# Performance work log

Hardware: AMD Instinct MI355X
Metric: run time of the kernel (lower is better)

The kernel has to match this reference:

```python
import jax, jax.numpy as jnp
import numpy as np

B, T, D = 2, 2048, 2048
N, K, H = 8, 4, 256
WINDOW = 1024
BASE_FREQ = 10000
ROPE_PROP = 1.0
SCALE_FACTOR = 1.0
K_MASK = -2.3819763e+38


def apply_rope(inputs, positions, base_frequency, scale_factor=1.0, rope_proportion=1.0):
    # inputs: [B,L,N,H], positions: [B,L]
    head_dim = inputs.shape[-1]
    rope_angles = int(rope_proportion * head_dim // 2)
    nope_angles = head_dim // 2 - rope_angles
    freq_exponents = 2.0 / head_dim * jnp.arange(rope_angles, dtype=jnp.float32)
    timescale = jnp.pad(base_frequency ** freq_exponents, (0, nope_angles),
                        mode='constant', constant_values=(0, jnp.inf))
    sinusoid = positions[..., None].astype(jnp.float32) / timescale[None, None, :]
    sinusoid = sinusoid[..., None, :] / scale_factor  # [B,L,1,H//2]
    sin = jnp.sin(sinusoid)
    cos = jnp.cos(sinusoid)
    first, second = jnp.split(inputs, 2, axis=-1)
    out = jnp.concatenate([first * cos - second * sin,
                           second * cos + first * sin], axis=-1)
    return out.astype(inputs.dtype)


def rms_norm(x, scale, eps=1e-6):
    var = jnp.mean(jnp.square(x.astype(jnp.float32)), axis=-1, keepdims=True)
    normed = x * jax.lax.rsqrt(var + eps)
    return (normed * (1.0 + scale)).astype(x.dtype)


def setup_inputs() -> dict:
    key = jax.random.key(0)
    ks = jax.random.split(key, 5)
    std = 0.02
    return {
        'x': jax.random.normal(ks[0], (B, T, D), jnp.float32),
        'positions': jnp.broadcast_to(jnp.arange(T, dtype=jnp.int32), (B, T)),
        'q_w': jax.random.normal(ks[1], (N, D, H), jnp.float32) * std,
        'k_w': jax.random.normal(ks[2], (K, D, H), jnp.float32) * std,
        'v_w': jax.random.normal(ks[3], (K, D, H), jnp.float32) * std,
        'o_w': jax.random.normal(ks[4], (N, H, D), jnp.float32) * std,
        'q_norm_scale': jnp.zeros((H,), jnp.float32),
        'k_norm_scale': jnp.zeros((H,), jnp.float32),
    }


def reference(x, positions, q_w, k_w, v_w, o_w, q_norm_scale, k_norm_scale):
    # QKV projections (Einsum modules)
    q = jnp.einsum('btd,ndh->btnh', x, q_w)   # [B,T,N,H]
    k = jnp.einsum('bsd,kdh->bskh', x, k_w)   # [B,S,K,H]
    v = jnp.einsum('bsd,kdh->bskh', x, v_w)
    # QK RMSNorm (gemma-style, zero-centered scale)
    q = rms_norm(q, q_norm_scale)
    k = rms_norm(k, k_norm_scale)
    # RoPE (local attention: base 10000, full proportion)
    q = apply_rope(q, positions, BASE_FREQ, SCALE_FACTOR, ROPE_PROP)
    k = apply_rope(k, positions, BASE_FREQ, SCALE_FACTOR, ROPE_PROP)
    q = q * (H ** -0.5)
    # GQA: group queries over kv heads
    G = N // K
    qg = q.reshape(B, T, K, G, H)
    logits = jnp.einsum('btkgh,bskh->btkgs', qg, k)  # [B,T,K,G,S]
    # causal + sliding-window mask from positions
    qp = positions[:, :, None]
    kp = positions[:, None, :]
    mask = (kp <= qp) & (kp > qp - WINDOW)           # [B,T,S]
    logits = jnp.where(mask[:, :, None, None, :], logits, K_MASK)
    probs = jax.nn.softmax(logits.astype(jnp.float32), axis=-1).astype(logits.dtype)
    out = jnp.einsum('btkgs,bskh->btkgh', probs, v).reshape(B, T, N, H)
    return jnp.einsum('btnh,nhd->btd', out, o_w)
```

## Files before the change

kernel.cpp:

```cpp
#include <hip/hip_runtime.h>
#include <cmath>

#define T_SEQ 2048
#define WINDOW 1024

typedef __attribute__((ext_vector_type(8))) short bf16x8;
typedef __attribute__((ext_vector_type(4))) float f32x4;
typedef __attribute__((ext_vector_type(16))) float f32x16;

__device__ __forceinline__ unsigned short f2bf(float f) {
  union { float f; unsigned int u; } v; v.f = f;
  unsigned int r = v.u + 0x7FFFu + ((v.u >> 16) & 1u);
  return (unsigned short)(r >> 16);
}
__device__ __forceinline__ float bf2f(unsigned short u) {
  union { unsigned int i; float f; } v; v.i = ((unsigned int)u) << 16;
  return v.f;
}

#define GLD16(gp, lp)                                                  \
  __builtin_amdgcn_global_load_lds(                                    \
      (__attribute__((address_space(1))) unsigned int*)(gp),           \
      (__attribute__((address_space(3))) unsigned int*)(lp), 16, 0, 0)

__global__ __launch_bounds__(256) void prep(
    const float* __restrict__ x,
    const float* __restrict__ qw, const float* __restrict__ kw,
    const float* __restrict__ vw, const float* __restrict__ ow,
    unsigned short* __restrict__ xb, unsigned short* __restrict__ wqkvt,
    unsigned short* __restrict__ wot) {
  __shared__ float tile[64][65];
  const int blk = blockIdx.x;
  const int tid = threadIdx.x;
  if (blk < 8192) {
    size_t i = (size_t)blk * 256 + tid;
    float4 v = *(const float4*)&x[i * 4];
    ushort4 o;
    o.x = f2bf(v.x); o.y = f2bf(v.y); o.z = f2bf(v.z); o.w = f2bf(v.w);
    *(ushort4*)&xb[i * 4] = o;
    return;
  }
  int tx = tid & 15, ty = tid >> 4;
  if (blk < 10240) {
    int idx = blk - 8192;
    int c0 = (idx & 63) * 64, d0 = (idx >> 6) * 64;
    const float* src; int hbase;
    if (c0 < 2048) { src = qw + (size_t)(c0 >> 8) * 524288; hbase = c0 & 255; }
    else if (c0 < 3072) { int cc = c0 - 2048; src = kw + (size_t)(cc >> 8) * 524288; hbase = cc & 255; }
    else { int cc = c0 - 3072; src = vw + (size_t)(cc >> 8) * 524288; hbase = cc & 255; }
#pragma unroll
    for (int p = 0; p < 4; ++p) {
      float4 v = *(const float4*)&src[(size_t)(d0 + ty + 16 * p) * 256 + hbase + tx * 4];
      tile[ty + 16 * p][tx * 4 + 0] = v.x; tile[ty + 16 * p][tx * 4 + 1] = v.y;
      tile[ty + 16 * p][tx * 4 + 2] = v.z; tile[ty + 16 * p][tx * 4 + 3] = v.w;
    }
    __syncthreads();
#pragma unroll
    for (int p = 0; p < 4; ++p) {
      int hh = ty + 16 * p;
      ushort4 o;
      o.x = f2bf(tile[tx * 4 + 0][hh]); o.y = f2bf(tile[tx * 4 + 1][hh]);
      o.z = f2bf(tile[tx * 4 + 2][hh]); o.w = f2bf(tile[tx * 4 + 3][hh]);
      *(ushort4*)&wqkvt[(size_t)(c0 + hh) * 2048 + d0 + tx * 4] = o;
    }
  } else {
    int idx = blk - 10240;
    int j0 = (idx & 31) * 64, d0 = (idx >> 5) * 64;
#pragma unroll
    for (int p = 0; p < 4; ++p) {
      float4 v = *(const float4*)&ow[(size_t)(j0 + ty + 16 * p) * 2048 + d0 + tx * 4];
      tile[ty + 16 * p][tx * 4 + 0] = v.x; tile[ty + 16 * p][tx * 4 + 1] = v.y;
      tile[ty + 16 * p][tx * 4 + 2] = v.z; tile[ty + 16 * p][tx * 4 + 3] = v.w;
    }
    __syncthreads();
#pragma unroll
    for (int p = 0; p < 4; ++p) {
      int hh = ty + 16 * p;
      ushort4 o;
      o.x = f2bf(tile[tx * 4 + 0][hh]); o.y = f2bf(tile[tx * 4 + 1][hh]);
      o.z = f2bf(tile[tx * 4 + 2][hh]); o.w = f2bf(tile[tx * 4 + 3][hh]);
      *(ushort4*)&wot[(size_t)(d0 + hh) * 2048 + j0 + tx * 4] = o;
    }
  }
}

__global__ __launch_bounds__(512) void gemm_qkv_256(
    const unsigned short* __restrict__ xb, const unsigned short* __restrict__ wt,
    unsigned short* __restrict__ qo, unsigned short* __restrict__ ko,
    unsigned short* __restrict__ vo) {
  __shared__ unsigned short lds[65536];
  const int tid = threadIdx.x;
  const int wave = tid >> 6, lane = tid & 63;
  const int wr = wave >> 2, wc = wave & 3;
  const int fm = lane & 15, fk = lane >> 4;

  const int bid = blockIdx.x;
  const int swz = (bid & 7) * 32 + (bid >> 3);
  const int m0 = (swz >> 4) * 256, n0 = (swz & 15) * 256;

  const int soff = fm * 32 + ((fk ^ ((fm >> 2) & 3)) << 3);
  const int aoff = wr * 4096 + soff;
  const int boff = wc * 2048 + soff;

  const unsigned short* Ab = xb + (size_t)m0 * 2048;
  const unsigned short* Bb = wt + (size_t)n0 * 2048;

  const int l0 = tid, l1 = tid + 512;
  const int r0 = l0 >> 2, o0 = l0 & 3;
  const int r1 = l1 >> 2, o1 = l1 & 3;
  const int sA0 = r0 * 2048 + ((o0 ^ ((r0 >> 2) & 3)) << 3);
  const int sA1 = r1 * 2048 + ((o1 ^ ((r1 >> 2) & 3)) << 3);

#define STAGE(srcbase, kofs, dstbase)                  \
  do {                                                 \
    GLD16((srcbase) + sA0 + (kofs), (dstbase) + l0 * 8); \
    GLD16((srcbase) + sA1 + (kofs), (dstbase) + l1 * 8); \
  } while (0)

  f32x4 acc[8][4];
#pragma unroll
  for (int i = 0; i < 8; ++i)
#pragma unroll
    for (int j = 0; j < 4; ++j) acc[i][j] = {0.f, 0.f, 0.f, 0.f};

  STAGE(Ab, 0,  lds + 0);
  STAGE(Bb, 0,  lds + 16384);
  STAGE(Ab, 32, lds + 8192);
  STAGE(Bb, 32, lds + 24576);
  STAGE(Ab, 64, lds + 32768);
  STAGE(Bb, 64, lds + 49152);
  asm volatile("s_waitcnt vmcnt(8)" ::: "memory");
  __builtin_amdgcn_s_barrier();

  for (int t = 0; t < 32; ++t) {
    const int p = t & 1;
    unsigned short* base = lds + p * 32768;
    unsigned short* xbase = lds + (p ^ 1) * 32768;
    const int t1 = (t < 31) ? t + 1 : 31;
    const int t2 = (t < 30) ? t + 2 : 31;

    bf16x8 a[4], b[4];
#pragma unroll
    for (int i = 0; i < 4; ++i) a[i] = *(const bf16x8*)(base + aoff + i * 512);
#pragma unroll
    for (int j = 0; j < 4; ++j) b[j] = *(const bf16x8*)(base + 16384 + boff + j * 512);
    STAGE(Ab, t1 * 64 + 32, xbase + 8192);
    __builtin_amdgcn_s_barrier();
    asm volatile("s_waitcnt lgkmcnt(0)" ::: "memory");
    __builtin_amdgcn_sched_barrier(0);
    __builtin_amdgcn_s_setprio(1);
#pragma unroll
    for (int i = 0; i < 4; ++i)
#pragma unroll
      for (int j = 0; j < 4; ++j)
        acc[i][j] = __builtin_amdgcn_mfma_f32_16x16x32_bf16(a[i], b[j], acc[i][j], 0, 0, 0);
    __builtin_amdgcn_s_setprio(0);
    __builtin_amdgcn_s_barrier();

#pragma unroll
    for (int i = 0; i < 4; ++i) a[i] = *(const bf16x8*)(base + aoff + (i + 4) * 512);
    STAGE(Bb, t1 * 64 + 32, xbase + 24576);
    __builtin_amdgcn_s_barrier();
    asm volatile("s_waitcnt lgkmcnt(0)" ::: "memory");
    __builtin_amdgcn_sched_barrier(0);
    __builtin_amdgcn_s_setprio(1);
#pragma unroll
    for (int i = 0; i < 4; ++i)
#pragma unroll
      for (int j = 0; j < 4; ++j)
        acc[i + 4][j] = __builtin_amdgcn_mfma_f32_16x16x32_bf16(a[i], b[j], acc[i + 4][j], 0, 0, 0);
    __builtin_amdgcn_s_setprio(0);
    asm volatile("s_waitcnt vmcnt(8)" ::: "memory");
    __builtin_amdgcn_s_barrier();

#pragma unroll
    for (int i = 0; i < 4; ++i) a[i] = *(const bf16x8*)(base + 8192 + aoff + i * 512);
#pragma unroll
    for (int j = 0; j < 4; ++j) b[j] = *(const bf16x8*)(base + 24576 + boff + j * 512);
    STAGE(Ab, t2 * 64, base + 0);
    __builtin_amdgcn_s_barrier();
    asm volatile("s_waitcnt lgkmcnt(0)" ::: "memory");
    __builtin_amdgcn_sched_barrier(0);
    __builtin_amdgcn_s_setprio(1);
#pragma unroll
    for (int i = 0; i < 4; ++i)
#pragma unroll
      for (int j = 0; j < 4; ++j)
        acc[i][j] = __builtin_amdgcn_mfma_f32_16x16x32_bf16(a[i], b[j], acc[i][j], 0, 0, 0);
    __builtin_amdgcn_s_setprio(0);
    __builtin_amdgcn_s_barrier();

#pragma unroll
    for (int i = 0; i < 4; ++i) a[i] = *(const bf16x8*)(base + 8192 + aoff + (i + 4) * 512);
    STAGE(Bb, t2 * 64, base + 16384);
    __builtin_amdgcn_s_barrier();
    asm volatile("s_waitcnt lgkmcnt(0)" ::: "memory");
    __builtin_amdgcn_sched_barrier(0);
    __builtin_amdgcn_s_setprio(1);
#pragma unroll
    for (int i = 0; i < 4; ++i)
#pragma unroll
      for (int j = 0; j < 4; ++j)
        acc[i + 4][j] = __builtin_amdgcn_mfma_f32_16x16x32_bf16(a[i], b[j], acc[i + 4][j], 0, 0, 0);
    __builtin_amdgcn_s_setprio(0);
    asm volatile("s_waitcnt vmcnt(8)" ::: "memory");
    __builtin_amdgcn_s_barrier();
  }
#undef STAGE

  unsigned short* obase; int ldo, cb;
  if (n0 < 2048) { obase = qo; ldo = 2048; cb = n0; }
  else if (n0 < 3072) { obase = ko; ldo = 1024; cb = n0 - 2048; }
  else { obase = vo; ldo = 1024; cb = n0 - 3072; }
  const int rbase = m0 + wr * 128 + (lane >> 4) * 4;
  const int cbase = cb + wc * 64 + fm;
#pragma unroll
  for (int i = 0; i < 8; ++i)
#pragma unroll
    for (int j = 0; j < 4; ++j)
#pragma unroll
      for (int r = 0; r < 4; ++r)
        obase[(size_t)(rbase + i * 16 + r) * ldo + cbase + j * 16] = f2bf(acc[i][j][r]);
}

__device__ __forceinline__ void gemm128_core(
    const unsigned short* __restrict__ A, const unsigned short* __restrict__ Bt,
    unsigned short* As, unsigned short* Bs, int m0, int n0, int K,
    f32x4 acc[4][4]) {
  const int tid = threadIdx.x;
  const int wave = tid >> 6, lane = tid & 63;
  const int wm = (wave & 1) << 6, wn = (wave >> 1) << 6;
  const int i0 = wave * 2, i1 = wave * 2 + 1;
  const int sr = lane >> 2;
  const int sc = (lane & 3) * 8;
  const size_t ar0 = (size_t)(m0 + i0 * 16 + sr) * K + sc;
  const size_t ar1 = (size_t)(m0 + i1 * 16 + sr) * K + sc;
  const size_t br0 = (size_t)(n0 + i0 * 16 + sr) * K + sc;
  const size_t br1 = (size_t)(n0 + i1 * 16 + sr) * K + sc;
  const int fm = lane & 15, fk = (lane >> 4) * 8;

  for (int kt = 0; kt < K; kt += 32) {
    GLD16(A + ar0 + kt, As + i0 * 512);
    GLD16(A + ar1 + kt, As + i1 * 512);
    GLD16(Bt + br0 + kt, Bs + i0 * 512);
    GLD16(Bt + br1 + kt, Bs + i1 * 512);
    __syncthreads();
    bf16x8 af[4], bv[4];
#pragma unroll
    for (int i = 0; i < 4; ++i)
      af[i] = *(const bf16x8*)&As[(wm + i * 16 + fm) * 32 + fk];
#pragma unroll
    for (int j = 0; j < 4; ++j)
      bv[j] = *(const bf16x8*)&Bs[(wn + j * 16 + fm) * 32 + fk];
#pragma unroll
    for (int i = 0; i < 4; ++i)
#pragma unroll
      for (int j = 0; j < 4; ++j)
        acc[i][j] = __builtin_amdgcn_mfma_f32_16x16x32_bf16(af[i], bv[j], acc[i][j], 0, 0, 0);
    __syncthreads();
  }
}

__global__ __launch_bounds__(256) void gemm_out_bf16(
    const unsigned short* __restrict__ ab, const unsigned short* __restrict__ wot,
    float* __restrict__ out) {
  __shared__ unsigned short As[128 * 32];
  __shared__ unsigned short Bs[128 * 32];
  const int n0 = blockIdx.x * 128, m0 = blockIdx.y * 128;
  f32x4 acc[4][4];
#pragma unroll
  for (int i = 0; i < 4; ++i)
#pragma unroll
    for (int j = 0; j < 4; ++j) acc[i][j] = {0.f, 0.f, 0.f, 0.f};
  gemm128_core(ab, wot, As, Bs, m0, n0, 2048, acc);

  const int lane = threadIdx.x & 63, wave = threadIdx.x >> 6;
  const int wm = (wave & 1) << 6, wn = (wave >> 1) << 6;
  const int rbase = m0 + wm + (lane >> 4) * 4;
  const int cbase = n0 + wn + (lane & 15);
#pragma unroll
  for (int i = 0; i < 4; ++i)
#pragma unroll
    for (int j = 0; j < 4; ++j)
#pragma unroll
      for (int r = 0; r < 4; ++r)
        out[(size_t)(rbase + i * 16 + r) * 2048 + cbase + j * 16] = acc[i][j][r];
}

__global__ __launch_bounds__(256) void postproc(
    unsigned short* __restrict__ qb, const unsigned short* __restrict__ kb,
    unsigned short* __restrict__ kpan,
    const unsigned short* __restrict__ vbf, unsigned short* __restrict__ vpan,
    const int* __restrict__ positions,
    const float* __restrict__ qns, const float* __restrict__ kns) {
  const int blk = blockIdx.x;
  const int tid = threadIdx.x;
  if (blk < 12288) {
    int row = blk * 4 + (tid >> 6);
    int lane = tid & 63;
    const unsigned short* src; const float* ns; float extra; int bt;
    bool isq = row < 32768;
    if (isq) {
      src = qb + (size_t)row * 256; ns = qns; extra = 0.0625f; bt = row >> 3;
    } else {
      int r = row - 32768;
      src = kb + (size_t)r * 256; ns = kns; extra = 1.0f; bt = r >> 2;
    }
    int pos = positions[bt];

    ushort4 u = *(const ushort4*)&src[lane << 2];
    float xv[4] = {bf2f(u.x), bf2f(u.y), bf2f(u.z), bf2f(u.w)};
    float ss = xv[0]*xv[0] + xv[1]*xv[1] + xv[2]*xv[2] + xv[3]*xv[3];
#pragma unroll
    for (int off = 1; off < 64; off <<= 1) ss += __shfl_xor(ss, off, 64);
    float rinv = rsqrtf(ss * (1.0f / 256.0f) + 1e-6f);

    float4 sc4 = *(const float4*)&ns[lane << 2];
    xv[0] *= rinv * (1.0f + sc4.x);
    xv[1] *= rinv * (1.0f + sc4.y);
    xv[2] *= rinv * (1.0f + sc4.z);
    xv[3] *= rinv * (1.0f + sc4.w);

    float ov[4];
#pragma unroll
    for (int c = 0; c < 4; ++c) ov[c] = __shfl_xor(xv[c], 32, 64);

    int hr = (lane & 31) << 2;
    float sgn = (lane < 32) ? -1.0f : 1.0f;
    ushort4 w4;
    unsigned short res[4];
#pragma unroll
    for (int c = 0; c < 4; ++c) {
      float invts = exp2f(-(float)(hr + c) * 0.10381025296523007f);
      float angle = (float)pos * invts;
      float sn, cs;
      __sincosf(angle, &sn, &cs);
      res[c] = f2bf((xv[c] * cs + sgn * ov[c] * sn) * extra);
    }
    w4.x = res[0]; w4.y = res[1]; w4.z = res[2]; w4.w = res[3];
    if (isq) {
      *(ushort4*)&qb[(size_t)row * 256 + (lane << 2)] = w4;
    } else {
      int r = row - 32768;
      int kvh = r & 3;
      int b_ = bt >> 11, t = bt & 2047;
      unsigned short* pan = kpan + (((size_t)(b_ * 4 + kvh) * 64 + (t >> 5)) * 8192);
      int s = t & 31;
      int c = lane >> 1;
      size_t el = (size_t)s * 256 + (size_t)((c ^ s) & 31) * 8 + (lane & 1) * 4;
      *(ushort4*)&pan[el] = w4;
    }
    return;
  }
  __shared__ unsigned short tile[64][68];
  int idx = blk - 12288;
  int h0 = (idx & 3) * 64;
  int t0 = ((idx >> 2) & 31) * 64;
  int z = idx >> 7;
  int tx = tid & 15, ty = tid >> 4;
  const unsigned short* src = vbf + ((size_t)(z >> 2) * 8192 + (z & 3)) * 256;
#pragma unroll
  for (int p = 0; p < 4; ++p) {
    ushort4 v = *(const ushort4*)&src[(size_t)(t0 + ty + 16 * p) * 1024 + h0 + tx * 4];
    tile[ty + 16 * p][tx * 4 + 0] = v.x; tile[ty + 16 * p][tx * 4 + 1] = v.y;
    tile[ty + 16 * p][tx * 4 + 2] = v.z; tile[ty + 16 * p][tx * 4 + 3] = v.w;
  }
  __syncthreads();
#pragma unroll
  for (int p = 0; p < 4; ++p) {
    int hh = ty + 16 * p;
    int h = h0 + hh;
    int t = t0 + tx * 4;
    int pp = t >> 5, s = t & 31;
    ushort4 o;
    o.x = tile[tx * 4 + 0][hh]; o.y = tile[tx * 4 + 1][hh];
    o.z = tile[tx * 4 + 2][hh]; o.w = tile[tx * 4 + 3][hh];
    size_t el = ((size_t)z * 64 + pp) * 8192 + (size_t)h * 32 +
                (size_t)(((s >> 3) ^ h ^ (h >> 2)) & 3) * 8 + (s & 7);
    *(ushort4*)&vpan[el] = o;
  }
}

__global__ __launch_bounds__(256) void attn_mfma(
    const unsigned short* __restrict__ qb,
    const unsigned short* __restrict__ kpan,
    const unsigned short* __restrict__ vpan,
    unsigned short* __restrict__ ob) {
  __shared__ __align__(16) unsigned short Kl[2][8192];
  __shared__ __align__(16) unsigned short Vl[2][8192];
  __shared__ __align__(16) unsigned short Ps[6144];

  const int tid = threadIdx.x;
  const int w = tid >> 6, lane = tid & 63;
  const int l5 = lane >> 5, l31 = lane & 31;
  const int pair = blockIdx.x & 7;
  const int t0 = (blockIdx.x >> 3) * 64;
  const int kvh = pair >> 1, b = pair & 1;
  const int n = 2 * kvh + (w & 1);
  const int tmin = t0 + (w >> 1) * 32, tmax = tmin + 31;

  bf16x8 aq[16];
  {
    const unsigned short* qrow =
        qb + (((size_t)b * 2048 + tmin + l31) * 8 + n) * 256 + l5 * 8;
#pragma unroll
    for (int kc = 0; kc < 16; ++kc) aq[kc] = *(const bf16x8*)(qrow + kc * 16);
  }

  f32x16 O[8], lsum;
#pragma unroll
  for (int i = 0; i < 8; ++i)
#pragma unroll
    for (int r = 0; r < 16; ++r) O[i][r] = 0.f;
#pragma unroll
  for (int r = 0; r < 16; ++r) lsum[r] = 0.f;

  bf16x8 ones;
#pragma unroll
  for (int i = 0; i < 8; ++i) ones[i] = (short)0x3F80;

  const unsigned short* kpb = kpan + (size_t)(b * 4 + kvh) * 64 * 8192;
  const unsigned short* vpb = vpan + (size_t)(b * 4 + kvh) * 64 * 8192;

  int s_lo = t0 - 1024; if (s_lo < 0) s_lo = 0;
  const int nt = ((t0 + 64) - s_lo) >> 5;

  {
    const unsigned short* kp = kpb + (size_t)(s_lo >> 5) * 8192;
    const unsigned short* vp = vpb + (size_t)(s_lo >> 5) * 8192;
#pragma unroll
    for (int j = 0; j < 4; ++j) { int g = (j * 256 + tid) * 8; GLD16(kp + g, &Kl[0][g]); }
#pragma unroll
    for (int j = 0; j < 4; ++j) { int g = (j * 256 + tid) * 8; GLD16(vp + g, &Vl[0][g]); }
  }

  for (int it = 0; it < nt; ++it) {
    const int cur = it & 1;
    const int s0 = s_lo + it * 32;
    if (it + 1 < nt) {
      const unsigned short* kp = kpb + ((size_t)(s0 >> 5) + 1) * 8192;
      const unsigned short* vp = vpb + ((size_t)(s0 >> 5) + 1) * 8192;
#pragma unroll
      for (int j = 0; j < 4; ++j) { int g = (j * 256 + tid) * 8; GLD16(kp + g, &Kl[cur ^ 1][g]); }
#pragma unroll
      for (int j = 0; j < 4; ++j) { int g = (j * 256 + tid) * 8; GLD16(vp + g, &Vl[cur ^ 1][g]); }
      asm volatile("s_waitcnt vmcnt(8)" ::: "memory");
    } else {
      asm volatile("s_waitcnt vmcnt(0)" ::: "memory");
    }
    __builtin_amdgcn_s_barrier();
    __builtin_amdgcn_sched_barrier(0);

    if ((s0 <= tmax) && (s0 + 31 >= tmin - 1023)) {
      const unsigned short* Kc = Kl[cur];
      const unsigned short* Vc = Vl[cur];

      f32x16 pa, pb;
#pragma unroll
      for (int r = 0; r < 16; ++r) { pa[r] = 0.f; pb[r] = 0.f; }
#pragma unroll
      for (int kc = 0; kc < 16; kc += 2) {
        bf16x8 b0 = *(const bf16x8*)&Kc[l31 * 256 + (((kc * 2 + l5) ^ l31) & 31) * 8];
        bf16x8 b1 = *(const bf16x8*)&Kc[l31 * 256 + ((((kc + 1) * 2 + l5) ^ l31) & 31) * 8];
        pa = __builtin_amdgcn_mfma_f32_32x32x16_bf16(aq[kc], b0, pa, 0, 0, 0);
        pb = __builtin_amdgcn_mfma_f32_32x32x16_bf16(aq[kc + 1], b1, pb, 0, 0, 0);
      }

      bool allvalid = (s0 + 31 <= tmin) && (s0 >= tmax - 1023);
      int scol = s0 + l31;
#pragma unroll
      for (int r = 0; r < 16; ++r) {
        float sv = pa[r] + pb[r];
        float p = exp2f(sv * 1.442695040888963f);
        int m = (r & 3) + 8 * (r >> 2) + 4 * l5;
        if (!allvalid) {
          int dt = (tmin + m) - scol;
          p = (dt >= 0 && dt < 1024) ? p : 0.f;
        }
        Ps[w * 1536 + (l31 >> 4) * 768 + m * 24 + (l31 & 15)] = f2bf(p);
      }

      bf16x8 pf0 = *(const bf16x8*)&Ps[w * 1536 + l31 * 24 + l5 * 8];
      bf16x8 pf1 = *(const bf16x8*)&Ps[w * 1536 + 768 + l31 * 24 + l5 * 8];
      lsum = __builtin_amdgcn_mfma_f32_32x32x16_bf16(pf0, ones, lsum, 0, 0, 0);
      lsum = __builtin_amdgcn_mfma_f32_32x32x16_bf16(pf1, ones, lsum, 0, 0, 0);
#pragma unroll
      for (int hb = 0; hb < 8; ++hb) {
        int row = hb * 32 + l31;
        int gh = (row ^ (row >> 2)) & 3;
        bf16x8 v0 = *(const bf16x8*)&Vc[row * 32 + ((l5 ^ gh) & 3) * 8];
        bf16x8 v1 = *(const bf16x8*)&Vc[row * 32 + (((2 + l5) ^ gh) & 3) * 8];
        O[hb] = __builtin_amdgcn_mfma_f32_32x32x16_bf16(pf0, v0, O[hb], 0, 0, 0);
        O[hb] = __builtin_amdgcn_mfma_f32_32x32x16_bf16(pf1, v1, O[hb], 0, 0, 0);
      }
    }
    asm volatile("s_waitcnt lgkmcnt(0)" ::: "memory");
    __builtin_amdgcn_sched_barrier(0);
    __builtin_amdgcn_s_barrier();
  }

  unsigned short* obase = ob + (((size_t)b * 2048 + tmin) * 8 + n) * 256;
#pragma unroll
  for (int r = 0; r < 16; ++r) {
    int m = (r & 3) + 8 * (r >> 2) + 4 * l5;
    float rinv = 1.0f / lsum[r];
    size_t rowoff = (size_t)m * 2048;
#pragma unroll
    for (int hb = 0; hb < 8; ++hb)
      obase[rowoff + hb * 32 + l31] = f2bf(O[hb][r] * rinv);
  }
}

extern "C" void kernel_launch(void* const* d_in, const int* in_sizes, int n_in,
                              void* d_out, int out_size, void* d_ws, size_t ws_size,
                              hipStream_t stream) {
  const float* x   = (const float*)d_in[0];
  const int* pos   = (const int*)d_in[1];
  const float* q_w = (const float*)d_in[2];
  const float* k_w = (const float*)d_in[3];
  const float* v_w = (const float*)d_in[4];
  const float* o_w = (const float*)d_in[5];
  const float* qns = (const float*)d_in[6];
  const float* kns = (const float*)d_in[7];
  float* out = (float*)d_out;

  unsigned short* W = (unsigned short*)d_ws;
  unsigned short* qb0   = W;
  unsigned short* kb0   = W + 8388608;
  unsigned short* vbf   = W + 12582912;
  unsigned short* vpan  = W + 16777216;
  unsigned short* kpan  = W + 20971520;
  unsigned short* xb    = W + 25165824;
  unsigned short* wqkvt = W + 33554432;
  unsigned short* abuf  = wqkvt;
  unsigned short* wot   = W + 41943040;

  prep<<<dim3(11264), 256, 0, stream>>>(x, q_w, k_w, v_w, o_w, xb, wqkvt, wot);
  gemm_qkv_256<<<dim3(256), 512, 0, stream>>>(xb, wqkvt, qb0, kb0, vbf);
  postproc<<<dim3(13312), 256, 0, stream>>>(qb0, kb0, kpan, vbf, vpan, pos, qns, kns);
  attn_mfma<<<dim3(256), 256, 0, stream>>>(qb0, kpan, vpan, abuf);
  gemm_out_bf16<<<dim3(16, 32), 256, 0, stream>>>(abuf, wot, out);
}
```

Baseline: 357.4 us.

## Split attention KV range across wave pairs with LDS merge of partial outputs

Each attention block now handles 32 queries instead of 64, and the grid doubles to 512 blocks. Within a block, two wave pairs process disjoint halves of the key/value tiles. Their unnormalized partial outputs and row sums are then added through LDS before the store. This raises parallelism and drops the redundant K/V loads where waves skipped tiles outside their window. In exchange it loses the double-buffered prefetch (each iteration waits on vmcnt(0)), adds a merge step with extra barriers, and K/V tiles are shared by fewer queries.

```diff
diff --git a/kernel.cpp b/kernel.cpp
--- a/kernel.cpp
+++ b/kernel.cpp
@@ -386,18 +386,18 @@
     const unsigned short* __restrict__ kpan,
     const unsigned short* __restrict__ vpan,
     unsigned short* __restrict__ ob) {
-  __shared__ __align__(16) unsigned short Kl[2][8192];
-  __shared__ __align__(16) unsigned short Vl[2][8192];
+  __shared__ __align__(16) unsigned short KV[32768];
   __shared__ __align__(16) unsigned short Ps[6144];
 
   const int tid = threadIdx.x;
   const int w = tid >> 6, lane = tid & 63;
+  const int hi = w >> 1;
   const int l5 = lane >> 5, l31 = lane & 31;
   const int pair = blockIdx.x & 7;
-  const int t0 = (blockIdx.x >> 3) * 64;
+  const int t0 = (blockIdx.x >> 3) * 32;
   const int kvh = pair >> 1, b = pair & 1;
   const int n = 2 * kvh + (w & 1);
-  const int tmin = t0 + (w >> 1) * 32, tmax = tmin + 31;
+  const int tmin = t0, tmax = t0 + 31;
 
   bf16x8 aq[16];
   {
@@ -423,37 +423,37 @@
   const unsigned short* vpb = vpan + (size_t)(b * 4 + kvh) * 64 * 8192;
 
   int s_lo = t0 - 1024; if (s_lo < 0) s_lo = 0;
-  const int nt = ((t0 + 64) - s_lo) >> 5;
-
-  {
-    const unsigned short* kp = kpb + (size_t)(s_lo >> 5) * 8192;
-    const unsigned short* vp = vpb + (size_t)(s_lo >> 5) * 8192;
-#pragma unroll
-    for (int j = 0; j < 4; ++j) { int g = (j * 256 + tid) * 8; GLD16(kp + g, &Kl[0][g]); }
-#pragma unroll
-    for (int j = 0; j < 4; ++j) { int g = (j * 256 + tid) * 8; GLD16(vp + g, &Vl[0][g]); }
-  }
-
-  for (int it = 0; it < nt; ++it) {
-    const int cur = it & 1;
-    const int s0 = s_lo + it * 32;
-    if (it + 1 < nt) {
-      const unsigned short* kp = kpb + ((size_t)(s0 >> 5) + 1) * 8192;
-      const unsigned short* vp = vpb + ((size_t)(s0 >> 5) + 1) * 8192;
-#pragma unroll
-      for (int j = 0; j < 4; ++j) { int g = (j * 256 + tid) * 8; GLD16(kp + g, &Kl[cur ^ 1][g]); }
-#pragma unroll
-      for (int j = 0; j < 4; ++j) { int g = (j * 256 + tid) * 8; GLD16(vp + g, &Vl[cur ^ 1][g]); }
-      asm volatile("s_waitcnt vmcnt(8)" ::: "memory");
-    } else {
-      asm volatile("s_waitcnt vmcnt(0)" ::: "memory");
-    }
+  const int p_lo = s_lo >> 5;
+  const int nt = ((t0 + 32) - s_lo) >> 5;
+  const int nh = (nt + 1) >> 1;
+
+  for (int i = 0; i < nh; ++i) {
+    const int tB = nh + i;
+    {
+      const unsigned short* kp = kpb + (size_t)(p_lo + i) * 8192;
+      const unsigned short* vp = vpb + (size_t)(p_lo + i) * 8192;
+#pragma unroll
+      for (int j = 0; j < 4; ++j) { int g = (j * 256 + tid) * 8; GLD16(kp + g, KV + g); }
+#pragma unroll
+      for (int j = 0; j < 4; ++j) { int g = (j * 256 + tid) * 8; GLD16(vp + g, KV + 16384 + g); }
+    }
+    if (tB < nt) {
+      const unsigned short* kp = kpb + (size_t)(p_lo + tB) * 8192;
+      const unsigned short* vp = vpb + (size_t)(p_lo + tB) * 8192;
+#pragma unroll
+      for (int j = 0; j < 4; ++j) { int g = (j * 256 + tid) * 8; GLD16(kp + g, KV + 8192 + g); }
+#pragma unroll
+      for (int j = 0; j < 4; ++j) { int g = (j * 256 + tid) * 8; GLD16(vp + g, KV + 24576 + g); }
+    }
+    asm volatile("s_waitcnt vmcnt(0)" ::: "memory");
     __builtin_amdgcn_s_barrier();
     __builtin_amdgcn_sched_barrier(0);
 
-    if ((s0 <= tmax) && (s0 + 31 >= tmin - 1023)) {
-      const unsigned short* Kc = Kl[cur];
-      const unsigned short* Vc = Vl[cur];
+    const int my = hi ? tB : i;
+    if (my < nt) {
+      const int s0 = s_lo + my * 32;
+      const unsigned short* Kc = KV + hi * 8192;
+      const unsigned short* Vc = KV + 16384 + hi * 8192;
 
       f32x16 pa, pb;
 #pragma unroll
@@ -499,15 +499,52 @@
     __builtin_amdgcn_s_barrier();
   }
 
-  unsigned short* obase = ob + (((size_t)b * 2048 + tmin) * 8 + n) * 256;
-#pragma unroll
-  for (int r = 0; r < 16; ++r) {
-    int m = (r & 3) + 8 * (r >> 2) + 4 * l5;
-    float rinv = 1.0f / lsum[r];
-    size_t rowoff = (size_t)m * 2048;
-#pragma unroll
-    for (int hb = 0; hb < 8; ++hb)
-      obase[rowoff + hb * 32 + l31] = f2bf(O[hb][r] * rinv);
+  float* scr = (float*)KV;
+  if (hi == 1) {
+    float* bb = scr + (w & 1) * 5184;
+#pragma unroll
+    for (int hb = 0; hb < 4; ++hb)
+#pragma unroll
+      for (int r = 0; r < 16; ++r) bb[lane * 81 + hb * 16 + r] = O[hb][r];
+#pragma unroll
+    for (int r = 0; r < 16; ++r) bb[lane * 81 + 64 + r] = lsum[r];
+  }
+  __syncthreads();
+  if (hi == 0) {
+    const float* bb = scr + (w & 1) * 5184;
+#pragma unroll
+    for (int hb = 0; hb < 4; ++hb)
+#pragma unroll
+      for (int r = 0; r < 16; ++r) O[hb][r] += bb[lane * 81 + hb * 16 + r];
+#pragma unroll
+    for (int r = 0; r < 16; ++r) lsum[r] += bb[lane * 81 + 64 + r];
+  }
+  __syncthreads();
+  if (hi == 1) {
+    float* bb = scr + (w & 1) * 4160;
+#pragma unroll
+    for (int hb = 4; hb < 8; ++hb)
+#pragma unroll
+      for (int r = 0; r < 16; ++r) bb[lane * 65 + (hb - 4) * 16 + r] = O[hb][r];
+  }
+  __syncthreads();
+  if (hi == 0) {
+    const float* bb = scr + (w & 1) * 4160;
+#pragma unroll
+    for (int hb = 4; hb < 8; ++hb)
+#pragma unroll
+      for (int r = 0; r < 16; ++r) O[hb][r] += bb[lane * 65 + (hb - 4) * 16 + r];
+
+    unsigned short* obase = ob + (((size_t)b * 2048 + tmin) * 8 + n) * 256;
+#pragma unroll
+    for (int r = 0; r < 16; ++r) {
+      int m = (r & 3) + 8 * (r >> 2) + 4 * l5;
+      float rinv = 1.0f / lsum[r];
+      size_t rowoff = (size_t)m * 2048;
+#pragma unroll
+      for (int hb = 0; hb < 8; ++hb)
+        obase[rowoff + hb * 32 + l31] = f2bf(O[hb][r] * rinv);
+    }
   }
 }
 
@@ -538,6 +575,6 @@
   prep<<<dim3(11264), 256, 0, stream>>>(x, q_w, k_w, v_w, o_w, xb, wqkvt, wot);
   gemm_qkv_256<<<dim3(256), 512, 0, stream>>>(xb, wqkvt, qb0, kb0, vbf);
   postproc<<<dim3(13312), 256, 0, stream>>>(qb0, kb0, kpan, vbf, vpan, pos, qns, kns);
-  attn_mfma<<<dim3(256), 256, 0, stream>>>(qb0, kpan, vpan, abuf);
+  attn_mfma<<<dim3(512), 256, 0, stream>>>(qb0, kpan, vpan, abuf);
   gemm_out_bf16<<<dim3(16, 32), 256, 0, stream>>>(abuf, wot, out);
 }
```

Result: no change. 351.8 us (-1.6%).
